# Optimization experiments

Measured on AMD Instinct MI355X. Metric: run time of the kernel, lower is better.

## Reference

```python
import jax, jax.numpy as jnp
import numpy as np

B, N, DIM = 4, 2048, 256
HEADS, CODEBOOK, HD = 4, 8192, 64  # HD = DIM // HEADS


def setup_inputs() -> dict:
    key = jax.random.key(0)
    k1, k2 = jax.random.split(key)
    x = jax.random.normal(k1, (B, N, DIM), dtype=jnp.float32)
    embed = jax.random.normal(k2, (HEADS, CODEBOOK, HD), dtype=jnp.float32)
    return {"x": x, "embed": embed}


def reference(x, embed):
    b, n, dim = x.shape
    h, c, d = embed.shape
    # 'b n (h d) -> h b n d' then pack to 'h (b n) d'
    flat = x.reshape(b, n, h, d).transpose(2, 0, 1, 3).reshape(h, b * n, d)
    x2 = jnp.sum(flat * flat, axis=-1)              # [h, bn]
    y2 = jnp.sum(embed * embed, axis=-1)            # [h, c]
    xy = jnp.einsum('hmd,hcd->hmc', flat, embed)    # [h, bn, c]
    sq = x2[:, :, None] + y2[:, None, :] - 2.0 * xy
    dist = -jnp.sqrt(jnp.maximum(sq, 0.0))          # clamp for fp safety
    embed_ind = jnp.argmax(dist, axis=-1)           # [h, bn]
    # gather codes per head
    quantize = jnp.take_along_axis(embed, embed_ind[:, :, None], axis=1)  # [h, bn, d]
    # 'h (b n) d -> b n (h d)'
    quantize = quantize.reshape(h, b, n, d).transpose(1, 2, 0, 3).reshape(b, n, h * d)
    # 'h (b n) -> b n h'
    embed_ind = embed_ind.reshape(h, b, n).transpose(1, 2, 0)
    return quantize, embed_ind
```

## Files before the change

### kernel.cpp

```cpp
#include <hip/hip_runtime.h>


#define HEADS    4
#define CODEBOOK 8192
#define HD       64
#define BQ       8192
#define QOFF     (4 * 2048 * 256)
#define NPART    8
#define CPART    (CODEBOOK / NPART)
#define SCODES   64
#define NSTAGE   (CPART / SCODES)
#define RSCALE   4096.0f
#define RINV     (1.0f / 4096.0f)

typedef _Float16 f16x8 __attribute__((ext_vector_type(8)));
typedef float    f32x4 __attribute__((ext_vector_type(4)));

__device__ _Float16 g_e0[HEADS * CODEBOOK * HD];
__device__ _Float16 g_e1[HEADS * CODEBOOK * HD];
__device__ float    g_y2[HEADS * CODEBOOK];
__device__ unsigned long long g_best[HEADS * BQ];
__device__ int                g_cnt[HEADS * 32];

__device__ inline void split2(float f, _Float16& h0, _Float16& h1) {
    h0 = (_Float16)f;
    float r = f - (float)h0;
    h1 = (_Float16)(r * RSCALE);
}

__device__ inline unsigned sortable(float v) {
    unsigned s = __float_as_uint(v);
    return s ^ ((s & 0x80000000u) ? 0xFFFFFFFFu : 0x80000000u);
}

__device__ inline void gl_lds16(const void* g, void* l) {
    __builtin_amdgcn_global_load_lds(
        (const __attribute__((address_space(1))) void*)g,
        (__attribute__((address_space(3))) void*)l, 16, 0, 0);
}

__global__ __launch_bounds__(256) void prep_kernel(const float* __restrict__ embed) {
    const int t   = threadIdx.x;
    const int row = blockIdx.x * 32 + (t >> 3);
    const int g   = t & 7;
    const float* p = embed + (size_t)row * HD + g * 8;
    float f[8];
    *reinterpret_cast<float4*>(&f[0]) = *reinterpret_cast<const float4*>(p);
    *reinterpret_cast<float4*>(&f[4]) = *reinterpret_cast<const float4*>(p + 4);
    f16x8 v0, v1;
    float ss = 0.f;
#pragma unroll
    for (int j = 0; j < 8; j++) {
        _Float16 h0, h1;
        split2(f[j], h0, h1);
        v0[j] = h0; v1[j] = h1;
        ss = fmaf(f[j], f[j], ss);
    }
    *reinterpret_cast<f16x8*>(&g_e0[(size_t)row * HD + g * 8]) = v0;
    *reinterpret_cast<f16x8*>(&g_e1[(size_t)row * HD + g * 8]) = v1;
#pragma unroll
    for (int off = 4; off >= 1; off >>= 1)
        ss += __shfl_xor(ss, off, 8);
    if (g == 0) g_y2[row] = -0.5f * ss;
}

__global__ __launch_bounds__(256, 2) void dist_kernel(const float* __restrict__ x,
                                                      const float* __restrict__ embed,
                                                      float* __restrict__ out) {
    __shared__ __align__(16) _Float16 tile[2][2][SCODES * HD];
    __shared__ int s_old;

    const int bid  = blockIdx.x;
    const int part = bid & 7;
    const int qg   = (bid >> 3) & 31;
    const int h    = bid >> 8;
    const int t    = threadIdx.x;
    const int wave = t >> 6;
    const int lane = t & 63;
    const int col  = lane & 15;
    const int quad = lane >> 4;

    const int qbase = qg * 256 + wave * 64;
    const int cbase = part * CPART;

    const int p  = wave & 1;
    const int hh = wave >> 1;
    const _Float16* eb   = p ? g_e1 : g_e0;
    const _Float16* gsrc = eb
        + ((size_t)(h * CODEBOOK + cbase + hh * 32 + (lane >> 3))) * HD
        + ((lane & 7) ^ (lane >> 3)) * 8;
    auto stage_issue = [&](int st, int buf) {
        const _Float16* src = gsrc + (size_t)st * (SCODES * HD);
#pragma unroll
        for (int i = 0; i < 4; i++)
            gl_lds16(src + i * 8 * HD, &tile[buf][p][(hh * 32 + i * 8) * HD]);
    };
    const float* y2p = g_y2 + h * CODEBOOK + cbase;

    stage_issue(0, 0);

    f16x8 a[4][2][2];
#pragma unroll
    for (int rt = 0; rt < 4; rt++) {
#pragma unroll
        for (int kh = 0; kh < 2; kh++) {
            const float* xp = x + ((size_t)(qbase + rt * 16 + col) * 256 + h * 64 + kh * 32 + quad * 8);
#pragma unroll
            for (int j = 0; j < 8; j++) {
                _Float16 h0, h1;
                split2(xp[j], h0, h1);
                a[rt][0][kh][j] = h0;
                a[rt][1][kh][j] = h1;
            }
        }
    }

    float bv[4][4]; int bc[4][4];
#pragma unroll
    for (int rt = 0; rt < 4; rt++)
#pragma unroll
        for (int r = 0; r < 4; r++) { bv[rt][r] = -3.4e38f; bc[rt][r] = 0; }

    __syncthreads();

    const int swbase = col & 7;
    const f32x4 z4 = {0.f, 0.f, 0.f, 0.f};

    for (int s = 0; s < NSTAGE; s++) {
        if (s + 1 < NSTAGE) stage_issue(s + 1, (s + 1) & 1);

#pragma unroll
        for (int inner = 0; inner < 4; inner++) {
            const int rbase = (inner * 16 + col) * HD;
            f16x8 b[2][2];
#pragma unroll
            for (int lvl = 0; lvl < 2; lvl++)
#pragma unroll
                for (int kh = 0; kh < 2; kh++)
                    b[lvl][kh] = *reinterpret_cast<const f16x8*>(
                        &tile[s & 1][lvl][rbase + ((((kh << 2) | quad) ^ swbase) << 3)]);

            const int   cl  = inner * 16 + col;
            const int   c   = s * SCODES + cl;
            const float ycn = y2p[c];
#pragma unroll
            for (int rt = 0; rt < 4; rt++) {
                __builtin_amdgcn_s_setprio(1);
                f32x4 aA = __builtin_amdgcn_mfma_f32_16x16x32_f16(a[rt][0][0], b[0][0], z4, 0, 0, 0);
                f32x4 aB = __builtin_amdgcn_mfma_f32_16x16x32_f16(a[rt][0][0], b[1][0], z4, 0, 0, 0);
                aB = __builtin_amdgcn_mfma_f32_16x16x32_f16(a[rt][1][0], b[0][0], aB, 0, 0, 0);
                aA = __builtin_amdgcn_mfma_f32_16x16x32_f16(a[rt][0][1], b[0][1], aA, 0, 0, 0);
                aB = __builtin_amdgcn_mfma_f32_16x16x32_f16(a[rt][0][1], b[1][1], aB, 0, 0, 0);
                aB = __builtin_amdgcn_mfma_f32_16x16x32_f16(a[rt][1][1], b[0][1], aB, 0, 0, 0);
                __builtin_amdgcn_s_setprio(0);
#pragma unroll
                for (int r = 0; r < 4; r++) {
                    float sv = fmaf(aB[r], RINV, aA[r] + ycn);
                    if (sv > bv[rt][r]) { bv[rt][r] = sv; bc[rt][r] = c; }
                }
            }
        }
        __syncthreads();
    }

#pragma unroll
    for (int rt = 0; rt < 4; rt++) {
#pragma unroll
        for (int r = 0; r < 4; r++) {
            float v = bv[rt][r]; int c = bc[rt][r];
#pragma unroll
            for (int off = 8; off >= 1; off >>= 1) {
                float ov = __shfl_xor(v, off, 16); int oc = __shfl_xor(c, off, 16);
                if (ov > v || (ov == v && oc < c)) { v = ov; c = oc; }
            }
            if (col == 0) {
                int q = h * BQ + qbase + rt * 16 + quad * 4 + r;
                unsigned long long pk =
                    ((unsigned long long)sortable(v) << 32) | (unsigned)(~(cbase + c));
                atomicMax(&g_best[q], pk);
            }
        }
    }

    const int grp = (h << 5) | qg;
    __syncthreads();
    if (t == 0) s_old = atomicAdd(&g_cnt[grp], 1);
    __syncthreads();
    if (s_old != NPART - 1) return;

    if (t == 0) atomicExch(&g_cnt[grp], 0);

    int* sidx = reinterpret_cast<int*>(tile);
    const int m0 = qg * 256;
    {
        const int q = h * BQ + m0 + t;
        unsigned long long pk = atomicAdd(&g_best[q], 0ull);
        int mc = (int)(~(unsigned)pk) & (CODEBOOK - 1);
        out[QOFF + (size_t)(m0 + t) * 4 + h] = (float)mc;
        sidx[t] = mc;
    }
    __syncthreads();

    const int rr = lane >> 4;
    const int fo = (lane & 15) * 4;
#pragma unroll
    for (int i = 0; i < 16; i++) {
        const int r   = wave * 64 + i * 4 + rr;
        const int idx = sidx[r];
        const float4 v = *reinterpret_cast<const float4*>(
            embed + ((size_t)h * CODEBOOK + idx) * HD + fo);
        *reinterpret_cast<float4*>(out + (size_t)(m0 + r) * 256 + h * 64 + fo) = v;
    }
}

extern "C" void kernel_launch(void* const* d_in, const int* in_sizes, int n_in,
                              void* d_out, int out_size, void* d_ws, size_t ws_size,
                              hipStream_t stream) {
    const float* x     = (const float*)d_in[0];
    const float* embed = (const float*)d_in[1];
    float*       out   = (float*)d_out;

    prep_kernel<<<1024, 256, 0, stream>>>(embed);
    dist_kernel<<<1024, 256, 0, stream>>>(x, embed, out);
}
```

Baseline: 176.6 us.

## Give each wave a private double-buffered codebook tile and drop block barriers

Before, all four waves loaded a shared 64-code tile per stage and synchronised with __syncthreads each stage. Now each wave loads the full 16-code tile it needs (both fp16 split levels) into its own LDS slice, double-buffered, and waits only on its own vmcnt/lgkmcnt, so there are no block-wide barriers in the main loop. y2 for the partition is also staged into LDS once up front. This removes barrier stalls and lets waves run independently, but it makes each wave fetch the whole codebook itself (four times the global/L2 traffic per block) with smaller, shallower prefetches, and it relies on hand-written waitcnt counts being correct.

Measured after the change: 190.5 us. 1.08x slower.

```diff
diff --git a/kernel.cpp b/kernel.cpp
--- a/kernel.cpp
+++ b/kernel.cpp
@@ -8,8 +8,9 @@
 #define QOFF     (4 * 2048 * 256)
 #define NPART    8
 #define CPART    (CODEBOOK / NPART)
-#define SCODES   64
-#define NSTAGE   (CPART / SCODES)
+#define MCODES   16
+#define NM       (CPART / MCODES)
+#define WTILE    (2 * 2 * MCODES * HD)
 #define RSCALE   4096.0f
 #define RINV     (1.0f / 4096.0f)
 
@@ -67,7 +68,8 @@
 __global__ __launch_bounds__(256, 2) void dist_kernel(const float* __restrict__ x,
                                                       const float* __restrict__ embed,
                                                       float* __restrict__ out) {
-    __shared__ __align__(16) _Float16 tile[2][2][SCODES * HD];
+    __shared__ __align__(16) _Float16 tile[4 * WTILE];
+    __shared__ float y2s[CPART];
     __shared__ int s_old;
 
     const int bid  = blockIdx.x;
@@ -83,21 +85,23 @@
     const int qbase = qg * 256 + wave * 64;
     const int cbase = part * CPART;
 
-    const int p  = wave & 1;
-    const int hh = wave >> 1;
-    const _Float16* eb   = p ? g_e1 : g_e0;
-    const _Float16* gsrc = eb
-        + ((size_t)(h * CODEBOOK + cbase + hh * 32 + (lane >> 3))) * HD
-        + ((lane & 7) ^ (lane >> 3)) * 8;
-    auto stage_issue = [&](int st, int buf) {
-        const _Float16* src = gsrc + (size_t)st * (SCODES * HD);
-#pragma unroll
-        for (int i = 0; i < 4; i++)
-            gl_lds16(src + i * 8 * HD, &tile[buf][p][(hh * 32 + i * 8) * HD]);
+    _Float16* wt = &tile[wave * WTILE];
+
+    const size_t pb = ((size_t)(h * CODEBOOK + cbase + (lane >> 3))) * HD
+                    + (size_t)(((lane & 7) ^ (lane >> 3)) * 8);
+    const _Float16* gs0 = g_e0 + pb;
+    const _Float16* gs1 = g_e1 + pb;
+    auto issue = [&](int st, int buf) {
+        const size_t o = (size_t)st * (MCODES * HD);
+        _Float16* d = wt + buf * (2 * MCODES * HD);
+        gl_lds16(gs0 + o,          d);
+        gl_lds16(gs0 + o + 8 * HD, d + 512);
+        gl_lds16(gs1 + o,          d + 1024);
+        gl_lds16(gs1 + o + 8 * HD, d + 1536);
     };
-    const float* y2p = g_y2 + h * CODEBOOK + cbase;
-
-    stage_issue(0, 0);
+
+    *reinterpret_cast<float4*>(&y2s[t * 4]) =
+        *reinterpret_cast<const float4*>(g_y2 + h * CODEBOOK + cbase + t * 4);
 
     f16x8 a[4][2][2];
 #pragma unroll
@@ -123,44 +127,48 @@
 
     __syncthreads();
 
-    const int swbase = col & 7;
+    issue(0, 0);
+    issue(1, 1);
+
+    const int o0 = ((quad ^ (col & 7)) << 3);
+    const int o1 = (((4 | quad) ^ (col & 7)) << 3);
+    const int colbase = col * HD;
     const f32x4 z4 = {0.f, 0.f, 0.f, 0.f};
 
-    for (int s = 0; s < NSTAGE; s++) {
-        if (s + 1 < NSTAGE) stage_issue(s + 1, (s + 1) & 1);
-
-#pragma unroll
-        for (int inner = 0; inner < 4; inner++) {
-            const int rbase = (inner * 16 + col) * HD;
-            f16x8 b[2][2];
-#pragma unroll
-            for (int lvl = 0; lvl < 2; lvl++)
-#pragma unroll
-                for (int kh = 0; kh < 2; kh++)
-                    b[lvl][kh] = *reinterpret_cast<const f16x8*>(
-                        &tile[s & 1][lvl][rbase + ((((kh << 2) | quad) ^ swbase) << 3)]);
-
-            const int   cl  = inner * 16 + col;
-            const int   c   = s * SCODES + cl;
-            const float ycn = y2p[c];
-#pragma unroll
-            for (int rt = 0; rt < 4; rt++) {
-                __builtin_amdgcn_s_setprio(1);
-                f32x4 aA = __builtin_amdgcn_mfma_f32_16x16x32_f16(a[rt][0][0], b[0][0], z4, 0, 0, 0);
-                f32x4 aB = __builtin_amdgcn_mfma_f32_16x16x32_f16(a[rt][0][0], b[1][0], z4, 0, 0, 0);
-                aB = __builtin_amdgcn_mfma_f32_16x16x32_f16(a[rt][1][0], b[0][0], aB, 0, 0, 0);
-                aA = __builtin_amdgcn_mfma_f32_16x16x32_f16(a[rt][0][1], b[0][1], aA, 0, 0, 0);
-                aB = __builtin_amdgcn_mfma_f32_16x16x32_f16(a[rt][0][1], b[1][1], aB, 0, 0, 0);
-                aB = __builtin_amdgcn_mfma_f32_16x16x32_f16(a[rt][1][1], b[0][1], aB, 0, 0, 0);
-                __builtin_amdgcn_s_setprio(0);
-#pragma unroll
-                for (int r = 0; r < 4; r++) {
-                    float sv = fmaf(aB[r], RINV, aA[r] + ycn);
-                    if (sv > bv[rt][r]) { bv[rt][r] = sv; bc[rt][r] = c; }
-                }
-            }
-        }
-        __syncthreads();
+    for (int m = 0; m < NM; m++) {
+        if (m < NM - 1) asm volatile("s_waitcnt vmcnt(4)" ::: "memory");
+        else            asm volatile("s_waitcnt vmcnt(0)" ::: "memory");
+
+        const _Float16* bp = wt + (m & 1) * (2 * MCODES * HD);
+        f16x8 b00 = *reinterpret_cast<const f16x8*>(&bp[colbase + o0]);
+        f16x8 b01 = *reinterpret_cast<const f16x8*>(&bp[colbase + o1]);
+        f16x8 b10 = *reinterpret_cast<const f16x8*>(&bp[1024 + colbase + o0]);
+        f16x8 b11 = *reinterpret_cast<const f16x8*>(&bp[1024 + colbase + o1]);
+
+        const int   c   = m * MCODES + col;
+        const float ycn = y2s[c];
+#pragma unroll
+        for (int rt = 0; rt < 4; rt++) {
+            __builtin_amdgcn_s_setprio(1);
+            f32x4 aA = __builtin_amdgcn_mfma_f32_16x16x32_f16(a[rt][0][0], b00, z4, 0, 0, 0);
+            f32x4 aB = __builtin_amdgcn_mfma_f32_16x16x32_f16(a[rt][0][0], b10, z4, 0, 0, 0);
+            aB = __builtin_amdgcn_mfma_f32_16x16x32_f16(a[rt][1][0], b00, aB, 0, 0, 0);
+            aA = __builtin_amdgcn_mfma_f32_16x16x32_f16(a[rt][0][1], b01, aA, 0, 0, 0);
+            aB = __builtin_amdgcn_mfma_f32_16x16x32_f16(a[rt][0][1], b11, aB, 0, 0, 0);
+            aB = __builtin_amdgcn_mfma_f32_16x16x32_f16(a[rt][1][1], b01, aB, 0, 0, 0);
+            __builtin_amdgcn_s_setprio(0);
+#pragma unroll
+            for (int r = 0; r < 4; r++) {
+                float sv = fmaf(aB[r], RINV, aA[r] + ycn);
+                if (sv > bv[rt][r]) { bv[rt][r] = sv; bc[rt][r] = c; }
+            }
+        }
+
+        if (m + 2 < NM) {
+            __builtin_amdgcn_sched_barrier(0);
+            asm volatile("s_waitcnt lgkmcnt(0)" ::: "memory");
+            issue(m + 2, m & 1);
+        }
     }
 
 #pragma unroll
```
